# Kernel tuning notes

Hardware: AMD Instinct MI355X
Metric: run time of the kernel (lower is better)

Reference implementation:

```python
import jax, jax.numpy as jnp
import numpy as np

B, T, D, O = 8, 128, 512, 512


def setup_inputs() -> dict:
    key = jax.random.key(0)
    ks = jax.random.split(key, 10)
    w = 0.02  # small init scale, mimics GlorotNormal magnitude
    return {
        "inputs": jax.random.normal(ks[0], (B, T, D), dtype=jnp.float32),
        "Wa": jax.random.normal(ks[1], (O, O), dtype=jnp.float32) * w,
        "Ua": jax.random.normal(ks[2], (D, O), dtype=jnp.float32) * w,
        "Va": jax.random.normal(ks[3], (O, 1), dtype=jnp.float32) * w,
        "Ba": jax.random.normal(ks[4], (1, O), dtype=jnp.float32) * w,
        "Wo": jax.random.normal(ks[5], (O, 1), dtype=jnp.float32) * w,
        "Uo": jax.random.normal(ks[6], (D, O), dtype=jnp.float32) * w,
        "Co": jax.random.normal(ks[7], (D, O), dtype=jnp.float32) * w,
        "Bo": jax.random.normal(ks[8], (1, O), dtype=jnp.float32) * w,
        "emb": jax.random.normal(ks[9], (O, O), dtype=jnp.float32) * w,
    }


def reference(inputs, Wa, Ua, Va, Ba, Wo, Uo, Co, Bo, emb):
    # inputs: [B,T,D]. Precompute loop-invariant attention keys (incl. Ba).
    UaH = jnp.einsum('btd,do->bto', inputs, Ua) + Ba  # [B,T,O]
    # GRU 'prev_state' arg at step t is inputs[:, t-1, :] (t=0 -> last step).
    prev_h = jnp.roll(inputs, 1, axis=1)              # [B,T,D]
    xs = jnp.swapaxes(prev_h, 0, 1)                   # [T,B,D]
    b, o = inputs.shape[0], Wa.shape[0]

    def step(prev_pred, h_prev):
        # --- attention cell (query = sigmoid(prev_pred)) ---
        s = jax.nn.sigmoid(prev_pred)                  # [B,O]
        WaS = s @ Wa                                   # [B,O]
        e = jnp.tanh(UaH + WaS[:, None, :])            # [B,T,O]
        scores = jnp.squeeze(e @ Va, -1)               # [B,T]
        sm = jax.nn.softmax(scores, axis=1)            # softmax over timesteps
        ctx = jnp.einsum('bt,btd->bd', sm, inputs)     # [B,D]
        # --- cascaded GRU cell ---
        emb_out = jax.nn.softmax(prev_pred, axis=-1) @ emb  # [B,O]
        WoY = emb_out @ Wo                             # [B,1] (broadcasts over O)
        pred = WoY + h_prev @ Uo + ctx @ Co + Bo       # [B,O]
        return pred, pred

    init = jnp.zeros((b, o), dtype=inputs.dtype)
    _, out = jax.lax.scan(step, init, xs)              # [T,B,O]
    return jnp.swapaxes(out, 0, 1)                     # [B,T,O]
```

## Files before the change

kernel.cpp:

```cpp
#include <hip/hip_runtime.h>

#define L2E 1.44269504088896340736f


typedef unsigned long long ull;

__device__ __forceinline__ void st_pack(ull* p, float v, int tag) {
  ull u = (((ull)(unsigned)tag) << 32) | (ull)__float_as_uint(v);
  __hip_atomic_store(p, u, __ATOMIC_RELAXED, __HIP_MEMORY_SCOPE_AGENT);
}
__device__ __forceinline__ ull ld_pack(const ull* p) {
  return __hip_atomic_load(p, __ATOMIC_RELAXED, __HIP_MEMORY_SCOPE_AGENT);
}
__device__ __forceinline__ unsigned bf16rne(float x) {
  unsigned u = __float_as_uint(x);
  return (u + 0x7FFFu + ((u >> 16) & 1u)) >> 16;
}

__global__ __launch_bounds__(256) void gemm_pre(
    const float* __restrict__ A, const float* __restrict__ Ua,
    const float* __restrict__ Uo, const float* __restrict__ Co,
    float* __restrict__ XW, unsigned* __restrict__ ICoB)
{
  __shared__ float sA[64][33];
  __shared__ float sB[32][68];
  const int r0 = blockIdx.x * 64;
  const int c0 = blockIdx.y * 64;
  const float* Wm; int cc0;
  if (c0 < 512)       { Wm = Ua; cc0 = c0; }
  else if (c0 < 1024) { Wm = Uo; cc0 = c0 - 512; }
  else                { Wm = Co; cc0 = c0 - 1024; }
  const int tid = threadIdx.x;
  const int ty4 = (tid >> 4) * 4;
  const int tx4 = (tid & 15) * 4;
  float acc[4][4] = {};
  for (int k0 = 0; k0 < 512; k0 += 32) {
    for (int t4 = tid; t4 < 512; t4 += 256) {
      int row = t4 >> 3, kq = (t4 & 7) << 2;
      float4 v = *reinterpret_cast<const float4*>(&A[(size_t)(r0 + row) * 512 + k0 + kq]);
      sA[row][kq] = v.x; sA[row][kq + 1] = v.y; sA[row][kq + 2] = v.z; sA[row][kq + 3] = v.w;
    }
    for (int t4 = tid; t4 < 512; t4 += 256) {
      int kk = t4 >> 4, cq = (t4 & 15) << 2;
      float4 v = *reinterpret_cast<const float4*>(&Wm[(size_t)(k0 + kk) * 512 + cc0 + cq]);
      sB[kk][cq] = v.x; sB[kk][cq + 1] = v.y; sB[kk][cq + 2] = v.z; sB[kk][cq + 3] = v.w;
    }
    __syncthreads();
    #pragma unroll 8
    for (int kk = 0; kk < 32; ++kk) {
      float a0 = sA[ty4 + 0][kk], a1 = sA[ty4 + 1][kk];
      float a2 = sA[ty4 + 2][kk], a3 = sA[ty4 + 3][kk];
      float4 bv = *reinterpret_cast<const float4*>(&sB[kk][tx4]);
      acc[0][0] += a0 * bv.x; acc[0][1] += a0 * bv.y; acc[0][2] += a0 * bv.z; acc[0][3] += a0 * bv.w;
      acc[1][0] += a1 * bv.x; acc[1][1] += a1 * bv.y; acc[1][2] += a1 * bv.z; acc[1][3] += a1 * bv.w;
      acc[2][0] += a2 * bv.x; acc[2][1] += a2 * bv.y; acc[2][2] += a2 * bv.z; acc[2][3] += a2 * bv.w;
      acc[3][0] += a3 * bv.x; acc[3][1] += a3 * bv.y; acc[3][2] += a3 * bv.z; acc[3][3] += a3 * bv.w;
    }
    __syncthreads();
  }
  if (c0 < 1024) {
    for (int i = 0; i < 4; ++i) {
      float4 v = make_float4(acc[i][0], acc[i][1], acc[i][2], acc[i][3]);
      *reinterpret_cast<float4*>(&XW[(size_t)(r0 + ty4 + i) * 1024 + c0 + tx4]) = v;
    }
  } else {
    const int ob = c0 - 1024 + tx4;
    for (int i = 0; i < 4; ++i) {
      int row = r0 + ty4 + i;
      unsigned w0 = bf16rne(acc[i][0]) | (bf16rne(acc[i][1]) << 16);
      unsigned w1 = bf16rne(acc[i][2]) | (bf16rne(acc[i][3]) << 16);
      uint2 w = make_uint2(w0, w1);
      *reinterpret_cast<uint2*>(&ICoB[(size_t)row * 256 + (ob >> 1)]) = w;
    }
  }
}

__global__ __launch_bounds__(512) void embwo_kernel(
    const float* __restrict__ emb, const float* __restrict__ Wo,
    float* __restrict__ gEmbWo)
{
  const int lane = threadIdx.x & 63;
  const int wv = threadIdx.x >> 6;
  const int kbase = blockIdx.x * 64 + wv * 8;
  for (int i = 0; i < 8; ++i) {
    const int k = kbase + i;
    float acc = 0.f;
    #pragma unroll
    for (int c = 0; c < 8; ++c) {
      int o = lane + 64 * c;
      acc += emb[(size_t)k * 512 + o] * Wo[o];
    }
    #pragma unroll
    for (int d = 1; d < 64; d <<= 1) acc += __shfl_xor(acc, d);
    if (lane == 0) gEmbWo[k] = acc;
  }
}

__global__ __launch_bounds__(256) void coop_scan(
    const float* __restrict__ Wa, const float* __restrict__ Va,
    const float* __restrict__ Ba, const float* __restrict__ Bo,
    const float* __restrict__ gXW, const unsigned* __restrict__ gICoB,
    const float* __restrict__ gEmbWo, ull* slotS64, float* __restrict__ out)
{
  extern __shared__ float smem[];
  float* sWa    = smem;
  float* sUaHT  = smem + 16384;
  float* sPred  = smem + 20512;
  float* sS     = smem + 21024;
  float* sEmb   = smem + 21536;
  float* sBo    = smem + 22048;
  float* sP1row = smem + 22560;
  float* sSm    = smem + 23072;
  float* sRedB  = smem + 23200;
  float* sRed   = smem + 23456;
  float* sVa    = smem + 23472;
  float* sWaS   = smem + 23504;

  const int tid = threadIdx.x;
  const int lane = tid & 63;
  const int wv = tid >> 6;
  const int b = blockIdx.x & 7;
  const int j = blockIdx.x >> 3;
  const int obase = j * 32;
  const int u = tid;

  for (int idx = tid; idx < 512 * 32; idx += 256) {
    int k = idx >> 5, oo = idx & 31;
    sWa[idx] = Wa[(size_t)k * 512 + obase + oo];
  }
  for (int idx = tid; idx < 128 * 32; idx += 256) {
    int tt = idx >> 5, oo = idx & 31;
    int col = obase + oo;
    sUaHT[oo * 129 + tt] = gXW[(size_t)(b * 128 + tt) * 1024 + col] + Ba[col];
  }
  if (tid < 32) sVa[tid] = Va[obase + tid];
  sEmb[tid] = gEmbWo[tid];       sEmb[tid + 256] = gEmbWo[tid + 256];
  sBo[tid]  = Bo[tid];           sBo[tid + 256]  = Bo[tid + 256];
  sPred[tid] = 0.f;              sPred[tid + 256] = 0.f;

  const unsigned* myICo = gICoB + (size_t)b * 32768;

  for (int t = 0; t < 128; ++t) {
    __syncthreads();

    float p1 = sPred[tid], p2 = sPred[tid + 256];
    sS[tid]       = 1.f / (1.f + exp2f(-p1 * L2E));
    sS[tid + 256] = 1.f / (1.f + exp2f(-p2 * L2E));
    {
      const int tprev = (t + 127) & 127;
      const float* uorow = gXW + (size_t)(b * 128 + tprev) * 1024 + 512;
      sP1row[tid]       = uorow[tid] + sBo[tid];
      sP1row[tid + 256] = uorow[tid + 256] + sBo[tid + 256];
    }
    float e1 = exp2f(p1 * L2E), e2 = exp2f(p2 * L2E);
    float Ep = e1 + e2;
    float Dp = e1 * sEmb[tid] + e2 * sEmb[tid + 256];
    #pragma unroll
    for (int d = 1; d < 64; d <<= 1) { Ep += __shfl_xor(Ep, d); Dp += __shfl_xor(Dp, d); }
    if (lane == 0) { sRed[wv] = Ep; sRed[4 + wv] = Dp; }
    __syncthreads();
    const float WoY = (sRed[4] + sRed[5] + sRed[6] + sRed[7])
                    / (sRed[0] + sRed[1] + sRed[2] + sRed[3]);

    {
      const int o = tid & 31, kg = tid >> 5, kb = kg * 64;
      float acc = 0.f;
      #pragma unroll 16
      for (int i = 0; i < 64; ++i) acc += sS[kb + i] * sWa[(kb + i) * 32 + o];
      sRedB[kg * 32 + o] = acc;
    }
    __syncthreads();
    if (tid < 32) {
      float w = 0.f;
      #pragma unroll
      for (int g = 0; g < 8; ++g) w += sRedB[g * 32 + tid];
      sWaS[tid] = w;
    }
    __syncthreads();

    {
      const int h = tid & 1, tp = tid >> 1;
      float acc = 0.f;
      #pragma unroll
      for (int i = 0; i < 16; ++i) {
        const int oo = h * 16 + i;
        float uu = sUaHT[oo * 129 + tp] + sWaS[oo];
        float ex = exp2f(uu * (2.f * L2E));
        acc += (1.f - 2.f / (1.f + ex)) * sVa[oo];
      }
      acc += __shfl_xor(acc, 1);
      if (h == 0)
        st_pack(slotS64 + (((t & 1) * 8 + b) * 16 + j) * 128 + tp, acc, t + 1);
    }

    if (tid < 128) {
      const ull* basep = slotS64 + ((t & 1) * 8 + b) * 2048 + tid;
      const unsigned want = (unsigned)(t + 1);
      float sc = 0.f;
      unsigned mask = 0xFFFFu;
      while (mask) {
        #pragma unroll
        for (int jj = 0; jj < 16; ++jj) {
          if (mask & (1u << jj)) {
            ull v = ld_pack(basep + jj * 128);
            if ((unsigned)(v >> 32) == want) {
              sc += __uint_as_float((unsigned)v);
              mask &= ~(1u << jj);
            }
          }
        }
      }
      float ev = exp2f(sc * L2E);
      sSm[tid] = ev;
      float sv = ev;
      #pragma unroll
      for (int d = 1; d < 64; d <<= 1) sv += __shfl_xor(sv, d);
      if (lane == 0) sRed[8 + wv] = sv;
    }
    __syncthreads();
    const float rden = 1.f / (sRed[8] + sRed[9]);

    {
      float a0 = 0.f, a1 = 0.f;
      const unsigned* col = myICo + u;
      #pragma unroll 8
      for (int tt = 0; tt < 128; ++tt) {
        float s = sSm[tt];
        unsigned w = col[(size_t)tt * 256];
        a0 = fmaf(s, __uint_as_float(w << 16), a0);
        a1 = fmaf(s, __uint_as_float(w & 0xFFFF0000u), a1);
      }
      float pred0 = WoY + sP1row[2 * u]     + a0 * rden;
      float pred1 = WoY + sP1row[2 * u + 1] + a1 * rden;
      sPred[2 * u]     = pred0;
      sPred[2 * u + 1] = pred1;
      if (u >= (obase >> 1) && u < (obase >> 1) + 16) {
        *reinterpret_cast<float2*>(&out[((size_t)(b * 128 + t)) * 512 + 2 * u]) =
            make_float2(pred0, pred1);
      }
    }
  }
}

extern "C" void kernel_launch(void* const* d_in, const int* in_sizes, int n_in,
                              void* d_out, int out_size, void* d_ws, size_t ws_size,
                              hipStream_t stream)
{
  const float* inputs = (const float*)d_in[0];
  const float* Wa  = (const float*)d_in[1];
  const float* Ua  = (const float*)d_in[2];
  const float* Va  = (const float*)d_in[3];
  const float* Ba  = (const float*)d_in[4];
  const float* Wo  = (const float*)d_in[5];
  const float* Uo  = (const float*)d_in[6];
  const float* Co  = (const float*)d_in[7];
  const float* Bo  = (const float*)d_in[8];
  const float* emb = (const float*)d_in[9];
  float* out = (float*)d_out;

  char* ws = (char*)d_ws;
  ull*      slotS64 = (ull*)(ws + 0);
  float*    gEmbWo  = (float*)(ws + 262144);
  unsigned* gICoB   = (unsigned*)(ws + 264192);
  float*    gXW     = (float*)(ws + 1313792);

  dim3 gg(16, 24);
  gemm_pre<<<gg, 256, 0, stream>>>(inputs, Ua, Uo, Co, gXW, gICoB);
  embwo_kernel<<<8, 512, 0, stream>>>(emb, Wo, gEmbWo);

  const int smem_bytes = 23536 * 4;
  hipFuncSetAttribute((const void*)coop_scan,
                      hipFuncAttributeMaxDynamicSharedMemorySize, smem_bytes);
  coop_scan<<<128, 256, smem_bytes, stream>>>(Wa, Va, Ba, Bo, gXW, gICoB,
                                              gEmbWo, slotS64, out);
}
```

Measured before the change: 1.365 ms.

## Keep per-batch bf16 inputs·Co matrix resident in registers across timesteps

Result: no change. 1.347 ms (-1.4%).

```diff
diff --git a/kernel.cpp b/kernel.cpp
--- a/kernel.cpp
+++ b/kernel.cpp
@@ -96,7 +96,7 @@
   }
 }
 
-__global__ __launch_bounds__(256) void coop_scan(
+__global__ __launch_bounds__(256, 1) void coop_scan(
     const float* __restrict__ Wa, const float* __restrict__ Va,
     const float* __restrict__ Ba, const float* __restrict__ Bo,
     const float* __restrict__ gXW, const unsigned* __restrict__ gICoB,
@@ -115,6 +115,7 @@
   float* sRed   = smem + 23456;
   float* sVa    = smem + 23472;
   float* sWaS   = smem + 23504;
+  float* sPP    = smem + 23536;
 
   const int tid = threadIdx.x;
   const int lane = tid & 63;
@@ -122,7 +123,6 @@
   const int b = blockIdx.x & 7;
   const int j = blockIdx.x >> 3;
   const int obase = j * 32;
-  const int u = tid;
 
   for (int idx = tid; idx < 512 * 32; idx += 256) {
     int k = idx >> 5, oo = idx & 31;
@@ -138,7 +138,14 @@
   sBo[tid]  = Bo[tid];           sBo[tid + 256]  = Bo[tid + 256];
   sPred[tid] = 0.f;              sPred[tid + 256] = 0.f;
 
-  const unsigned* myICo = gICoB + (size_t)b * 32768;
+  uint4 rIC[32];
+  {
+    const unsigned* basep = gICoB + (size_t)b * 32768
+                          + (size_t)(wv * 32) * 256 + lane * 4;
+    #pragma unroll
+    for (int i = 0; i < 32; ++i)
+      rIC[i] = *reinterpret_cast<const uint4*>(basep + (size_t)i * 256);
+  }
 
   for (int t = 0; t < 128; ++t) {
     __syncthreads();
@@ -221,21 +228,40 @@
     const float rden = 1.f / (sRed[8] + sRed[9]);
 
     {
-      float a0 = 0.f, a1 = 0.f;
-      const unsigned* col = myICo + u;
-      #pragma unroll 8
-      for (int tt = 0; tt < 128; ++tt) {
-        float s = sSm[tt];
-        unsigned w = col[(size_t)tt * 256];
-        a0 = fmaf(s, __uint_as_float(w << 16), a0);
-        a1 = fmaf(s, __uint_as_float(w & 0xFFFF0000u), a1);
-      }
-      float pred0 = WoY + sP1row[2 * u]     + a0 * rden;
-      float pred1 = WoY + sP1row[2 * u + 1] + a1 * rden;
-      sPred[2 * u]     = pred0;
-      sPred[2 * u + 1] = pred1;
-      if (u >= (obase >> 1) && u < (obase >> 1) + 16) {
-        *reinterpret_cast<float2*>(&out[((size_t)(b * 128 + t)) * 512 + 2 * u]) =
+      float a0 = 0.f, a1 = 0.f, a2 = 0.f, a3 = 0.f;
+      float a4 = 0.f, a5 = 0.f, a6 = 0.f, a7 = 0.f;
+      const int rbase = wv * 32;
+      #pragma unroll
+      for (int i = 0; i < 32; ++i) {
+        float s = sSm[rbase + i];
+        uint4 w = rIC[i];
+        a0 = fmaf(s, __uint_as_float(w.x << 16),         a0);
+        a1 = fmaf(s, __uint_as_float(w.x & 0xFFFF0000u), a1);
+        a2 = fmaf(s, __uint_as_float(w.y << 16),         a2);
+        a3 = fmaf(s, __uint_as_float(w.y & 0xFFFF0000u), a3);
+        a4 = fmaf(s, __uint_as_float(w.z << 16),         a4);
+        a5 = fmaf(s, __uint_as_float(w.z & 0xFFFF0000u), a5);
+        a6 = fmaf(s, __uint_as_float(w.w << 16),         a6);
+        a7 = fmaf(s, __uint_as_float(w.w & 0xFFFF0000u), a7);
+      }
+      float* pp = sPP + wv * 512 + lane * 8;
+      *reinterpret_cast<float4*>(pp)     = make_float4(a0, a1, a2, a3);
+      *reinterpret_cast<float4*>(pp + 4) = make_float4(a4, a5, a6, a7);
+    }
+    __syncthreads();
+    {
+      float v0 = 0.f, v1 = 0.f;
+      #pragma unroll
+      for (int w2 = 0; w2 < 4; ++w2) {
+        float2 q = *reinterpret_cast<const float2*>(&sPP[w2 * 512 + 2 * tid]);
+        v0 += q.x; v1 += q.y;
+      }
+      float pred0 = WoY + sP1row[2 * tid]     + v0 * rden;
+      float pred1 = WoY + sP1row[2 * tid + 1] + v1 * rden;
+      sPred[2 * tid]     = pred0;
+      sPred[2 * tid + 1] = pred1;
+      if (tid >= (obase >> 1) && tid < (obase >> 1) + 16) {
+        *reinterpret_cast<float2*>(&out[((size_t)(b * 128 + t)) * 512 + 2 * tid]) =
             make_float2(pred0, pred1);
       }
     }
@@ -268,7 +294,7 @@
   gemm_pre<<<gg, 256, 0, stream>>>(inputs, Ua, Uo, Co, gXW, gICoB);
   embwo_kernel<<<8, 512, 0, stream>>>(emb, Wo, gEmbWo);
 
-  const int smem_bytes = 23536 * 4;
+  const int smem_bytes = 25584 * 4;
   hipFuncSetAttribute((const void*)coop_scan,
                       hipFuncAttributeMaxDynamicSharedMemorySize, smem_bytes);
   coop_scan<<<128, 256, smem_bytes, stream>>>(Wa, Va, Ba, Bo, gXW, gICoB,
```
